# Kernel tuning notes

Measured on AMD Instinct MI355X. Metric: run time of the kernel, lower is better.

Reference implementation:

```python
import jax, jax.numpy as jnp
import numpy as np

N_NODES = 50000
N_EDGES = 800000
IN_F = 128
OUT_F = 128
EDGE_F = 6


def setup_inputs() -> dict:
    key = jax.random.key(0)
    k1, k2, k3, k4, k5, k6, k7 = jax.random.split(key, 7)
    nodeFeatures = jax.random.normal(k1, (N_NODES, IN_F), dtype=jnp.float32)
    edgeIndex = jax.random.randint(k2, (N_EDGES, 2), 0, N_NODES, dtype=jnp.int64)
    edgeFeatures = jax.random.normal(k3, (N_EDGES, EDGE_F), dtype=jnp.float32)
    # nn.Linear params (kaiming-uniform-ish init scale)
    lim_n = 1.0 / np.sqrt(IN_F)
    lim_e = 1.0 / np.sqrt(EDGE_F)
    W = jax.random.uniform(k4, (IN_F, OUT_F), minval=-lim_n, maxval=lim_n, dtype=jnp.float32)
    b = jax.random.uniform(k5, (OUT_F,), minval=-lim_n, maxval=lim_n, dtype=jnp.float32)
    We = jax.random.uniform(k6, (EDGE_F, OUT_F), minval=-lim_e, maxval=lim_e, dtype=jnp.float32)
    be = jax.random.uniform(k7, (OUT_F,), minval=-lim_e, maxval=lim_e, dtype=jnp.float32)
    return {"nodeFeatures": nodeFeatures, "edgeIndex": edgeIndex,
            "edgeFeatures": edgeFeatures, "W": W, "b": b, "We": We, "be": be}


def reference(nodeFeatures, edgeIndex, edgeFeatures, W, b, We, be):
    # node linear: [N, out]
    transformed = nodeFeatures @ W + b
    # edge linear: [E, out]
    edgeMsg = edgeFeatures @ We + be
    src = edgeIndex[:, 0]
    dst = edgeIndex[:, 1]
    # per-edge message = transformed[src] + edgeMsg, scatter-add into dst
    messages = transformed[src] + edgeMsg  # [E, out]
    aggregated = jax.ops.segment_sum(messages, dst, num_segments=nodeFeatures.shape[0])
    return jax.nn.relu(aggregated)
```

## Files before the change

kernel.cpp:

```cpp
#include <hip/hip_runtime.h>
#include <hip/hip_bf16.h>
#include <stdint.h>

#define IN_F 128
#define EDGE_F 6
#define TILE_E 4096
#define NBIN_PAD 256
#define BCAP 8192
#define IDXN 8192
#define CAST_B 400

using bf16x8 = __attribute__((ext_vector_type(8))) short;
using f32x4  = __attribute__((ext_vector_type(4))) float;

__device__ __forceinline__ float bf2f(unsigned short u) {
    return __uint_as_float(((unsigned int)u) << 16);
}
__device__ __forceinline__ unsigned short f2bfbits(float f) {
    __hip_bfloat16 h = __float2bfloat16(f);
    return *reinterpret_cast<unsigned short*>(&h);
}
__device__ __forceinline__ unsigned int packbf(float a, float b) {
    return ((unsigned int)f2bfbits(b) << 16) | (unsigned int)f2bfbits(a);
}

__global__ __launch_bounds__(256) void sort_pack_cast(
        const int* __restrict__ eidx, const float* __restrict__ ef,
        uint4* __restrict__ rec_c, unsigned short* __restrict__ pmat,
        unsigned short* __restrict__ lmat,
        int n_edges, int nblk_e, int n_cast, int n_nodes,
        const float* __restrict__ nf, unsigned short* __restrict__ nfb,
        const float* __restrict__ W, const float* __restrict__ b,
        const float* __restrict__ We, const float* __restrict__ be,
        unsigned short* __restrict__ Wpack, float* __restrict__ W2pack) {
    const int tid = threadIdx.x;
    const int blk = blockIdx.x;
    __shared__ unsigned int qxs[TILE_E];
    __shared__ int hist[NBIN_PAD];
    __shared__ int cur[NBIN_PAD];

    if (blk < nblk_e) {
        hist[tid] = 0;
        __syncthreads();
        const int e0 = blk * TILE_E;
        const int lim = min(TILE_E, n_edges - e0);
        for (int i = tid; i < lim; i += 256) {
            const int2 pr = reinterpret_cast<const int2*>(eidx)[e0 + i];
            const unsigned int q = (unsigned int)pr.x | ((unsigned int)pr.y << 16);
            qxs[i] = q;
            atomicAdd(&hist[q >> 24], 1);
        }
        __syncthreads();
        const int own = hist[tid];
        for (int off = 1; off < 256; off <<= 1) {
            int t2 = (tid >= off) ? hist[tid - off] : 0;
            __syncthreads();
            hist[tid] += t2;
            __syncthreads();
        }
        const int excl = hist[tid] - own;
        pmat[(size_t)blk * NBIN_PAD + tid] = (unsigned short)own;
        lmat[(size_t)blk * NBIN_PAD + tid] = (unsigned short)excl;
        cur[tid] = excl;
        __syncthreads();
        uint4* seg = rec_c + (size_t)blk * TILE_E;
        for (int i = tid; i < lim; i += 256) {
            const unsigned int q = qxs[i];
            const float2* efs = reinterpret_cast<const float2*>(ef + (size_t)(e0 + i) * EDGE_F);
            const float2 f0 = efs[0], f1 = efs[1], f2 = efs[2];
            uint4 r;
            r.x = q;
            r.y = packbf(f0.x, f0.y);
            r.z = packbf(f1.x, f1.y);
            r.w = packbf(f2.x, f2.y);
            const int pos = atomicAdd(&cur[q >> 24], 1);
            seg[pos] = r;
        }
    } else if (blk == nblk_e) {
        for (int idx = tid; idx < 16384; idx += 256) {
            int j = idx & 7, lane = (idx >> 3) & 63, ft = (idx >> 9) & 7, kb = idx >> 12;
            int k = kb * 32 + (lane >> 4) * 8 + j;
            int f = ft * 16 + (lane & 15);
            Wpack[idx] = f2bfbits(W[k * 128 + f]);
        }
        for (int idx = tid; idx < 1024; idx += 256) {
            int j = idx >> 7, f = idx & 127;
            float w = 0.f;
            if (j < 6)       w = We[j * 128 + f];
            else if (j == 6) w = b[f] + be[f];
            W2pack[idx] = w;
        }
        if (tid < 16) {
            uint4 z; z.x = z.y = z.z = z.w = 0u;
            reinterpret_cast<uint4*>(nfb + (size_t)n_nodes * IN_F)[tid] = z;
        }
    } else {
        const int cb = blk - nblk_e - 1;
        const int ncb = gridDim.x - nblk_e - 1;
        for (int i = cb * 256 + tid; i < n_cast; i += ncb * 256) {
            const float4 lo = reinterpret_cast<const float4*>(nf)[2 * i];
            const float4 hi = reinterpret_cast<const float4*>(nf)[2 * i + 1];
            uint4 o;
            o.x = packbf(lo.x, lo.y); o.y = packbf(lo.z, lo.w);
            o.z = packbf(hi.x, hi.y); o.w = packbf(hi.z, hi.w);
            reinterpret_cast<uint4*>(nfb)[i] = o;
        }
    }
}

__global__ __launch_bounds__(512) void fine_rank(
        const uint4* __restrict__ rec_c, const unsigned short* __restrict__ pmat,
        const unsigned short* __restrict__ lmat,
        uint4* __restrict__ rec, int2* __restrict__ pr2,
        int n_nodes, int nblk_e) {
    const int tid = threadIdx.x;
    const int c = blockIdx.x;
    __shared__ int rstart[NBIN_PAD + 1];
    __shared__ int rbaseg[NBIN_PAD];
    __shared__ int fcnt[256];
    __shared__ int fpos[256];
    __shared__ int idxl[IDXN];

    if (tid < 256) {
        const bool r = (tid < nblk_e);
        fcnt[tid] = r ? pmat[(size_t)tid * NBIN_PAD + c] : 0;
        rbaseg[tid] = tid * TILE_E + (r ? (int)lmat[(size_t)tid * NBIN_PAD + c] : 0);
    }
    __syncthreads();
    for (int off = 1; off < 256; off <<= 1) {
        int v = 0;
        if (tid < 256 && tid >= off) v = fcnt[tid - off];
        __syncthreads();
        if (tid < 256) fcnt[tid] += v;
        __syncthreads();
    }
    if (tid < 256) rstart[tid + 1] = fcnt[tid];
    if (tid == 0) rstart[0] = 0;
    __syncthreads();
    int sz = rstart[256];
    if (sz > IDXN) sz = IDXN;
    __syncthreads();
    if (tid < 256) fcnt[tid] = 0;
    __syncthreads();
    for (int base = 0; base < sz; base += 2048) {
        int ii[4], g[4];
        unsigned int qx[4];
#pragma unroll
        for (int u = 0; u < 4; ++u) ii[u] = base + u * 512 + tid;
#pragma unroll
        for (int u = 0; u < 4; ++u) {
            if (ii[u] < sz) {
                int lo = 0, hi = 255;
                while (lo < hi) {
                    const int mid = (lo + hi + 1) >> 1;
                    if (rstart[mid] <= ii[u]) lo = mid; else hi = mid - 1;
                }
                g[u] = rbaseg[lo] + (ii[u] - rstart[lo]);
                idxl[ii[u]] = g[u];
            }
        }
#pragma unroll
        for (int u = 0; u < 4; ++u)
            if (ii[u] < sz)
                qx[u] = reinterpret_cast<const unsigned int*>(rec_c)[(size_t)g[u] * 4];
#pragma unroll
        for (int u = 0; u < 4; ++u)
            if (ii[u] < sz) atomicAdd(&fcnt[(qx[u] >> 16) & 255], 1);
    }
    __syncthreads();
    int own = 0, ownp = 0, pexcl = 0;
    if (tid < 256) { own = fcnt[tid]; ownp = (own + 7) & ~7; fcnt[tid] = ownp; }
    __syncthreads();
    for (int off = 1; off < 256; off <<= 1) {
        int v = 0;
        if (tid < 256 && tid >= off) v = fcnt[tid - off];
        __syncthreads();
        if (tid < 256) fcnt[tid] += v;
        __syncthreads();
    }
    const size_t obase = (size_t)c * BCAP;
    if (tid < 256) {
        pexcl = fcnt[tid] - ownp;
        fpos[tid] = pexcl;
        const int n = c * 256 + tid;
        if (n < n_nodes) {
            int2 pr; pr.x = (int)(obase + pexcl); pr.y = own;
            pr2[n] = pr;
        }
    }
    __syncthreads();
    for (int base = 0; base < sz; base += 2048) {
        int ii[4];
        uint4 q[4];
#pragma unroll
        for (int u = 0; u < 4; ++u) ii[u] = base + u * 512 + tid;
#pragma unroll
        for (int u = 0; u < 4; ++u)
            if (ii[u] < sz) q[u] = rec_c[idxl[ii[u]]];
#pragma unroll
        for (int u = 0; u < 4; ++u) {
            if (ii[u] < sz) {
                const int r = atomicAdd(&fpos[(q[u].x >> 16) & 255], 1);
                if (r < BCAP) rec[obase + r] = q[u];
            }
        }
    }
    if (tid < 256) {
        uint4 dmy; dmy.x = (unsigned int)n_nodes; dmy.y = dmy.z = dmy.w = 0u;
        for (int j = own; j < ownp && pexcl + j < BCAP; ++j)
            rec[obase + pexcl + j] = dmy;
    }
}

__global__ __launch_bounds__(256) void aggregate_bf16(
        const unsigned short* __restrict__ nfb, const uint4* __restrict__ rec,
        const int2* __restrict__ pr2, unsigned short* __restrict__ S,
        unsigned short* __restrict__ E8, int n_nodes) {
    const int lane = threadIdx.x & 63;
    const int wv = __builtin_amdgcn_readfirstlane(threadIdx.x >> 6);
    const int n = blockIdx.x * 4 + wv;
    if (n >= n_nodes) return;
    const int2 pr = pr2[n];
    const int deg = pr.y;
    const int nb = (deg + 7) >> 3;
    const int half = lane >> 5;
    const int hl = lane & 31;
    float a0 = 0.f, a1 = 0.f, a2 = 0.f, a3 = 0.f;
    float e0 = 0.f, e1 = 0.f, e2 = 0.f, e3 = 0.f, e4 = 0.f, e5 = 0.f;
    int i = pr.x;
    for (int bb = 0; bb < nb; ++bb, i += 8) {
        uint4 q[8];
#pragma unroll
        for (int j = 0; j < 8; ++j) q[j] = rec[i + j];
        uint2 u[4];
#pragma unroll
        for (int p = 0; p < 4; ++p) {
            const unsigned int sA = q[2 * p].x & 0xFFFFu;
            const unsigned int sB = q[2 * p + 1].x & 0xFFFFu;
            const unsigned int s = half ? sB : sA;
            u[p] = reinterpret_cast<const uint2*>(nfb + (size_t)s * IN_F)[hl];
        }
#pragma unroll
        for (int p = 0; p < 4; ++p) {
            a0 += bf2f((unsigned short)u[p].x);
            a1 += bf2f((unsigned short)(u[p].x >> 16));
            a2 += bf2f((unsigned short)u[p].y);
            a3 += bf2f((unsigned short)(u[p].y >> 16));
        }
#pragma unroll
        for (int j = 0; j < 8; ++j) {
            e0 += bf2f((unsigned short)q[j].y);
            e1 += bf2f((unsigned short)(q[j].y >> 16));
            e2 += bf2f((unsigned short)q[j].z);
            e3 += bf2f((unsigned short)(q[j].z >> 16));
            e4 += bf2f((unsigned short)q[j].w);
            e5 += bf2f((unsigned short)(q[j].w >> 16));
        }
    }
    a0 += __shfl_xor(a0, 32, 64);
    a1 += __shfl_xor(a1, 32, 64);
    a2 += __shfl_xor(a2, 32, 64);
    a3 += __shfl_xor(a3, 32, 64);
    if (half == 0) {
        uint2 o;
        o.x = packbf(a0, a1);
        o.y = packbf(a2, a3);
        reinterpret_cast<uint2*>(S + (size_t)n * IN_F)[hl] = o;
    }
    if (lane == 0) {
        uint4 q;
        q.x = packbf(e0, e1);
        q.y = packbf(e2, e3);
        q.z = packbf(e4, e5);
        q.w = packbf((float)deg, 0.f);
        *reinterpret_cast<uint4*>(E8 + (size_t)n * 8) = q;
    }
}

__global__ __launch_bounds__(256) void gemm_mfma(
        const unsigned short* __restrict__ S, const unsigned short* __restrict__ E8,
        const unsigned short* __restrict__ Wpack, const float* __restrict__ W2pack,
        float* __restrict__ out, int n_nodes) {
    __shared__ __align__(16) short Wl[16384];
    __shared__ float W2l[1024];
    const int tid = threadIdx.x;
    for (int i = tid; i < 2048; i += 256)
        reinterpret_cast<uint4*>(Wl)[i] = reinterpret_cast<const uint4*>(Wpack)[i];
    for (int i = tid; i < 1024; i += 256) W2l[i] = W2pack[i];

    const int wv = tid >> 6, lane = tid & 63;
    const int m = lane & 15, quad = lane >> 4;
    const int n0 = blockIdx.x * 64 + wv * 16;

    const int arow = min(n0 + m, n_nodes - 1);
    const unsigned short* ap = S + (size_t)arow * IN_F + quad * 8;
    bf16x8 a[4];
#pragma unroll
    for (int kb = 0; kb < 4; ++kb)
        a[kb] = *reinterpret_cast<const bf16x8*>(ap + kb * 32);

    __syncthreads();

    f32x4 acc[8];
#pragma unroll
    for (int ft = 0; ft < 8; ++ft) acc[ft] = (f32x4){0.f, 0.f, 0.f, 0.f};

#pragma unroll
    for (int kb = 0; kb < 4; ++kb) {
#pragma unroll
        for (int ft = 0; ft < 8; ++ft) {
            const bf16x8 bfrag =
                reinterpret_cast<const bf16x8*>(Wl)[(kb * 8 + ft) * 64 + lane];
            acc[ft] = __builtin_amdgcn_mfma_f32_16x16x32_bf16(a[kb], bfrag, acc[ft], 0, 0, 0);
        }
    }

    float e[4][7];
#pragma unroll
    for (int r = 0; r < 4; ++r) {
        const int n = min(n0 + quad * 4 + r, n_nodes - 1);
        const uint4 q = *reinterpret_cast<const uint4*>(E8 + (size_t)n * 8);
        e[r][0] = bf2f((unsigned short)q.x); e[r][1] = bf2f((unsigned short)(q.x >> 16));
        e[r][2] = bf2f((unsigned short)q.y); e[r][3] = bf2f((unsigned short)(q.y >> 16));
        e[r][4] = bf2f((unsigned short)q.z); e[r][5] = bf2f((unsigned short)(q.z >> 16));
        e[r][6] = bf2f((unsigned short)q.w);
    }
    __syncthreads();
    float* So = reinterpret_cast<float*>(Wl);
#pragma unroll
    for (int ft = 0; ft < 8; ++ft) {
        const int f = ft * 16 + m;
        float w2[7];
#pragma unroll
        for (int j = 0; j < 7; ++j) w2[j] = W2l[j * 128 + f];
#pragma unroll
        for (int r = 0; r < 4; ++r) {
            float v = acc[ft][r];
#pragma unroll
            for (int j = 0; j < 7; ++j) v += e[r][j] * w2[j];
            So[(wv * 16 + quad * 4 + r) * 128 + f] = fmaxf(v, 0.f);
        }
    }
    __syncthreads();
    const size_t nb0 = (size_t)blockIdx.x * 64;
    for (int i = tid; i < 2048; i += 256) {
        const int row = i >> 5;
        if (nb0 + row < (size_t)n_nodes)
            reinterpret_cast<uint4*>(out)[(nb0 + row) * 32 + (i & 31)] =
                reinterpret_cast<const uint4*>(So)[i];
    }
}

extern "C" void kernel_launch(void* const* d_in, const int* in_sizes, int n_in,
                              void* d_out, int out_size, void* d_ws, size_t ws_size,
                              hipStream_t stream) {
    const float* nf = (const float*)d_in[0];
    const int* eidx = (const int*)d_in[1];
    const float* ef = (const float*)d_in[2];
    const float* W  = (const float*)d_in[3];
    const float* b  = (const float*)d_in[4];
    const float* We = (const float*)d_in[5];
    const float* be = (const float*)d_in[6];
    float* out = (float*)d_out;

    const int n_nodes = in_sizes[0] / IN_F;
    const int n_edges = in_sizes[1] / 2;

    const int nblk_e = (n_edges + TILE_E - 1) / TILE_E;
    const int nbin = (n_nodes + 255) >> 8;
    const int n_cast = n_nodes * (IN_F / 8);

    uint4* rec   = (uint4*)d_ws;
    uint4* rec_c = rec + (size_t)nbin * BCAP;
    unsigned short* S = (unsigned short*)(rec_c + (size_t)nblk_e * TILE_E);
    unsigned short* E8 = S + (size_t)n_nodes * IN_F;
    unsigned short* Wpack = E8 + (size_t)n_nodes * 8;
    float* W2pack = (float*)(Wpack + 16384);
    int2* pr2 = (int2*)(W2pack + 1024);
    unsigned short* pmat = (unsigned short*)(pr2 + n_nodes);
    unsigned short* lmat = pmat + (size_t)nblk_e * NBIN_PAD;
    unsigned short* nfb = lmat + (size_t)nblk_e * NBIN_PAD;

    sort_pack_cast<<<nblk_e + 1 + CAST_B, 256, 0, stream>>>(
        eidx, ef, rec_c, pmat, lmat, n_edges, nblk_e, n_cast, n_nodes,
        nf, nfb, W, b, We, be, Wpack, W2pack);
    fine_rank<<<nbin, 512, 0, stream>>>(rec_c, pmat, lmat, rec, pr2,
                                        n_nodes, nblk_e);
    aggregate_bf16<<<(n_nodes + 3) / 4, 256, 0, stream>>>(nfb, rec, pr2, S, E8, n_nodes);
    gemm_mfma<<<(n_nodes + 63) / 64, 256, 0, stream>>>(S, E8, Wpack, W2pack, out, n_nodes);
}
```

Measured before the change: 177.6 us.

## Split bf16 node table into four feature-quarter passes for cache-resident gathers

The bf16 node-feature table is stored as four column-quarter tables of 32 features each, and aggregation runs four passes, each gathering only one quarter. A single quarter table is a quarter of the full table's size, so the random source-row gathers are more likely to hit in L2/MALL. A compact 16-bit source-index array is also written so the later passes do not reread the 16-byte edge records; only pass 0 accumulates edge features. The cost is four times as many aggregate blocks, a repeated CSR walk with narrower 8-byte gathers per pass, a three-stage shuffle reduction, and extra index-array writes in the ranking kernel.

```diff
diff --git a/kernel.cpp b/kernel.cpp
--- a/kernel.cpp
+++ b/kernel.cpp
@@ -28,13 +28,14 @@
         const int* __restrict__ eidx, const float* __restrict__ ef,
         uint4* __restrict__ rec_c, unsigned short* __restrict__ pmat,
         unsigned short* __restrict__ lmat,
-        int n_edges, int nblk_e, int n_cast, int n_nodes,
-        const float* __restrict__ nf, unsigned short* __restrict__ nfb,
+        int n_edges, int nblk_e, int n_nodes,
+        const float* __restrict__ nf, unsigned short* __restrict__ nfbq,
         const float* __restrict__ W, const float* __restrict__ b,
         const float* __restrict__ We, const float* __restrict__ be,
         unsigned short* __restrict__ Wpack, float* __restrict__ W2pack) {
     const int tid = threadIdx.x;
     const int blk = blockIdx.x;
+    const size_t qstr = (size_t)(n_nodes + 1) * 32;
     __shared__ unsigned int qxs[TILE_E];
     __shared__ int hist[NBIN_PAD];
     __shared__ int cur[NBIN_PAD];
@@ -91,19 +92,29 @@
             W2pack[idx] = w;
         }
         if (tid < 16) {
+            const int q = tid >> 2, sub = tid & 3;
             uint4 z; z.x = z.y = z.z = z.w = 0u;
-            reinterpret_cast<uint4*>(nfb + (size_t)n_nodes * IN_F)[tid] = z;
+            *reinterpret_cast<uint4*>(nfbq + (size_t)q * qstr +
+                                      (size_t)n_nodes * 32 + sub * 8) = z;
         }
     } else {
         const int cb = blk - nblk_e - 1;
         const int ncb = gridDim.x - nblk_e - 1;
-        for (int i = cb * 256 + tid; i < n_cast; i += ncb * 256) {
-            const float4 lo = reinterpret_cast<const float4*>(nf)[2 * i];
-            const float4 hi = reinterpret_cast<const float4*>(nf)[2 * i + 1];
+        const int per_q = n_nodes * 4;
+        const int total = n_nodes * 16;
+        for (int i = cb * 256 + tid; i < total; i += ncb * 256) {
+            const int q = i / per_q;
+            const int rem = i - q * per_q;
+            const int node = rem >> 2, sub = rem & 3;
+            const float4 lo = *reinterpret_cast<const float4*>(
+                nf + (size_t)node * IN_F + q * 32 + sub * 8);
+            const float4 hi = *reinterpret_cast<const float4*>(
+                nf + (size_t)node * IN_F + q * 32 + sub * 8 + 4);
             uint4 o;
             o.x = packbf(lo.x, lo.y); o.y = packbf(lo.z, lo.w);
             o.z = packbf(hi.x, hi.y); o.w = packbf(hi.z, hi.w);
-            reinterpret_cast<uint4*>(nfb)[i] = o;
+            *reinterpret_cast<uint4*>(nfbq + (size_t)q * qstr +
+                                      (size_t)node * 32 + sub * 8) = o;
         }
     }
 }
@@ -111,8 +122,8 @@
 __global__ __launch_bounds__(512) void fine_rank(
         const uint4* __restrict__ rec_c, const unsigned short* __restrict__ pmat,
         const unsigned short* __restrict__ lmat,
-        uint4* __restrict__ rec, int2* __restrict__ pr2,
-        int n_nodes, int nblk_e) {
+        uint4* __restrict__ rec, unsigned short* __restrict__ srcp,
+        int2* __restrict__ pr2, int n_nodes, int nblk_e) {
     const int tid = threadIdx.x;
     const int c = blockIdx.x;
     __shared__ int rstart[NBIN_PAD + 1];
@@ -201,73 +212,79 @@
         for (int u = 0; u < 4; ++u) {
             if (ii[u] < sz) {
                 const int r = atomicAdd(&fpos[(q[u].x >> 16) & 255], 1);
-                if (r < BCAP) rec[obase + r] = q[u];
+                if (r < BCAP) {
+                    rec[obase + r] = q[u];
+                    srcp[obase + r] = (unsigned short)(q[u].x & 0xFFFFu);
+                }
             }
         }
     }
     if (tid < 256) {
         uint4 dmy; dmy.x = (unsigned int)n_nodes; dmy.y = dmy.z = dmy.w = 0u;
-        for (int j = own; j < ownp && pexcl + j < BCAP; ++j)
+        for (int j = own; j < ownp && pexcl + j < BCAP; ++j) {
             rec[obase + pexcl + j] = dmy;
+            srcp[obase + pexcl + j] = (unsigned short)n_nodes;
+        }
     }
 }
 
 __global__ __launch_bounds__(256) void aggregate_bf16(
-        const unsigned short* __restrict__ nfb, const uint4* __restrict__ rec,
-        const int2* __restrict__ pr2, unsigned short* __restrict__ S,
-        unsigned short* __restrict__ E8, int n_nodes) {
+        const unsigned short* __restrict__ nfbq, const uint4* __restrict__ rec,
+        const unsigned short* __restrict__ srcp, const int2* __restrict__ pr2,
+        unsigned short* __restrict__ Sq, unsigned short* __restrict__ E8,
+        int n_nodes, int nbn) {
     const int lane = threadIdx.x & 63;
     const int wv = __builtin_amdgcn_readfirstlane(threadIdx.x >> 6);
-    const int n = blockIdx.x * 4 + wv;
+    const int pass = blockIdx.x / nbn;
+    const int bi = blockIdx.x - pass * nbn;
+    const int n = bi * 4 + wv;
     if (n >= n_nodes) return;
+    const size_t qstr = (size_t)(n_nodes + 1) * 32;
+    const unsigned short* tab = nfbq + (size_t)pass * qstr;
     const int2 pr = pr2[n];
     const int deg = pr.y;
     const int nb = (deg + 7) >> 3;
-    const int half = lane >> 5;
-    const int hl = lane & 31;
-    float a0 = 0.f, a1 = 0.f, a2 = 0.f, a3 = 0.f;
+    const int es = lane >> 3;
+    const int fl = lane & 7;
+    float b0 = 0.f, b1 = 0.f, b2 = 0.f, b3 = 0.f;
     float e0 = 0.f, e1 = 0.f, e2 = 0.f, e3 = 0.f, e4 = 0.f, e5 = 0.f;
     int i = pr.x;
     for (int bb = 0; bb < nb; ++bb, i += 8) {
-        uint4 q[8];
-#pragma unroll
-        for (int j = 0; j < 8; ++j) q[j] = rec[i + j];
-        uint2 u[4];
-#pragma unroll
-        for (int p = 0; p < 4; ++p) {
-            const unsigned int sA = q[2 * p].x & 0xFFFFu;
-            const unsigned int sB = q[2 * p + 1].x & 0xFFFFu;
-            const unsigned int s = half ? sB : sA;
-            u[p] = reinterpret_cast<const uint2*>(nfb + (size_t)s * IN_F)[hl];
-        }
-#pragma unroll
-        for (int p = 0; p < 4; ++p) {
-            a0 += bf2f((unsigned short)u[p].x);
-            a1 += bf2f((unsigned short)(u[p].x >> 16));
-            a2 += bf2f((unsigned short)u[p].y);
-            a3 += bf2f((unsigned short)(u[p].y >> 16));
-        }
-#pragma unroll
-        for (int j = 0; j < 8; ++j) {
-            e0 += bf2f((unsigned short)q[j].y);
-            e1 += bf2f((unsigned short)(q[j].y >> 16));
-            e2 += bf2f((unsigned short)q[j].z);
-            e3 += bf2f((unsigned short)(q[j].z >> 16));
-            e4 += bf2f((unsigned short)q[j].w);
-            e5 += bf2f((unsigned short)(q[j].w >> 16));
-        }
-    }
-    a0 += __shfl_xor(a0, 32, 64);
-    a1 += __shfl_xor(a1, 32, 64);
-    a2 += __shfl_xor(a2, 32, 64);
-    a3 += __shfl_xor(a3, 32, 64);
-    if (half == 0) {
+        const int s = srcp[i + es];
+        const uint2 u = *reinterpret_cast<const uint2*>(tab + (size_t)s * 32 + fl * 4);
+        b0 += bf2f((unsigned short)u.x);
+        b1 += bf2f((unsigned short)(u.x >> 16));
+        b2 += bf2f((unsigned short)u.y);
+        b3 += bf2f((unsigned short)(u.y >> 16));
+        if (pass == 0) {
+            uint4 q[8];
+#pragma unroll
+            for (int j = 0; j < 8; ++j) q[j] = rec[i + j];
+#pragma unroll
+            for (int j = 0; j < 8; ++j) {
+                e0 += bf2f((unsigned short)q[j].y);
+                e1 += bf2f((unsigned short)(q[j].y >> 16));
+                e2 += bf2f((unsigned short)q[j].z);
+                e3 += bf2f((unsigned short)(q[j].z >> 16));
+                e4 += bf2f((unsigned short)q[j].w);
+                e5 += bf2f((unsigned short)(q[j].w >> 16));
+            }
+        }
+    }
+    b0 += __shfl_xor(b0, 8, 64);  b1 += __shfl_xor(b1, 8, 64);
+    b2 += __shfl_xor(b2, 8, 64);  b3 += __shfl_xor(b3, 8, 64);
+    b0 += __shfl_xor(b0, 16, 64); b1 += __shfl_xor(b1, 16, 64);
+    b2 += __shfl_xor(b2, 16, 64); b3 += __shfl_xor(b3, 16, 64);
+    b0 += __shfl_xor(b0, 32, 64); b1 += __shfl_xor(b1, 32, 64);
+    b2 += __shfl_xor(b2, 32, 64); b3 += __shfl_xor(b3, 32, 64);
+    if (es == 0) {
         uint2 o;
-        o.x = packbf(a0, a1);
-        o.y = packbf(a2, a3);
-        reinterpret_cast<uint2*>(S + (size_t)n * IN_F)[hl] = o;
-    }
-    if (lane == 0) {
+        o.x = packbf(b0, b1);
+        o.y = packbf(b2, b3);
+        *reinterpret_cast<uint2*>(Sq + (size_t)pass * n_nodes * 32 +
+                                  (size_t)n * 32 + fl * 4) = o;
+    }
+    if (pass == 0 && lane == 0) {
         uint4 q;
         q.x = packbf(e0, e1);
         q.y = packbf(e2, e3);
@@ -278,7 +295,7 @@
 }
 
 __global__ __launch_bounds__(256) void gemm_mfma(
-        const unsigned short* __restrict__ S, const unsigned short* __restrict__ E8,
+        const unsigned short* __restrict__ Sq, const unsigned short* __restrict__ E8,
         const unsigned short* __restrict__ Wpack, const float* __restrict__ W2pack,
         float* __restrict__ out, int n_nodes) {
     __shared__ __align__(16) short Wl[16384];
@@ -293,11 +310,11 @@
     const int n0 = blockIdx.x * 64 + wv * 16;
 
     const int arow = min(n0 + m, n_nodes - 1);
-    const unsigned short* ap = S + (size_t)arow * IN_F + quad * 8;
     bf16x8 a[4];
 #pragma unroll
     for (int kb = 0; kb < 4; ++kb)
-        a[kb] = *reinterpret_cast<const bf16x8*>(ap + kb * 32);
+        a[kb] = *reinterpret_cast<const bf16x8*>(
+            Sq + (size_t)kb * n_nodes * 32 + (size_t)arow * 32 + quad * 8);
 
     __syncthreads();
 
@@ -368,24 +385,26 @@
 
     const int nblk_e = (n_edges + TILE_E - 1) / TILE_E;
     const int nbin = (n_nodes + 255) >> 8;
-    const int n_cast = n_nodes * (IN_F / 8);
+    const int nbn = (n_nodes + 3) / 4;
 
     uint4* rec   = (uint4*)d_ws;
     uint4* rec_c = rec + (size_t)nbin * BCAP;
-    unsigned short* S = (unsigned short*)(rec_c + (size_t)nblk_e * TILE_E);
-    unsigned short* E8 = S + (size_t)n_nodes * IN_F;
+    unsigned short* E8 = (unsigned short*)(rec_c + (size_t)nblk_e * TILE_E);
     unsigned short* Wpack = E8 + (size_t)n_nodes * 8;
-    float* W2pack = (float*)(Wpack + 16384);
+    unsigned short* Sq = Wpack + 16384;
+    unsigned short* nfbq = Sq + (size_t)4 * n_nodes * 32;
+    unsigned short* srcp = nfbq + (size_t)4 * (n_nodes + 1) * 32;
+    unsigned short* pmat = srcp + (size_t)nbin * BCAP;
+    unsigned short* lmat = pmat + (size_t)nblk_e * NBIN_PAD;
+    float* W2pack = (float*)(lmat + (size_t)nblk_e * NBIN_PAD);
     int2* pr2 = (int2*)(W2pack + 1024);
-    unsigned short* pmat = (unsigned short*)(pr2 + n_nodes);
-    unsigned short* lmat = pmat + (size_t)nblk_e * NBIN_PAD;
-    unsigned short* nfb = lmat + (size_t)nblk_e * NBIN_PAD;
 
     sort_pack_cast<<<nblk_e + 1 + CAST_B, 256, 0, stream>>>(
-        eidx, ef, rec_c, pmat, lmat, n_edges, nblk_e, n_cast, n_nodes,
-        nf, nfb, W, b, We, be, Wpack, W2pack);
-    fine_rank<<<nbin, 512, 0, stream>>>(rec_c, pmat, lmat, rec, pr2,
+        eidx, ef, rec_c, pmat, lmat, n_edges, nblk_e, n_nodes,
+        nf, nfbq, W, b, We, be, Wpack, W2pack);
+    fine_rank<<<nbin, 512, 0, stream>>>(rec_c, pmat, lmat, rec, srcp, pr2,
                                         n_nodes, nblk_e);
-    aggregate_bf16<<<(n_nodes + 3) / 4, 256, 0, stream>>>(nfb, rec, pr2, S, E8, n_nodes);
-    gemm_mfma<<<(n_nodes + 63) / 64, 256, 0, stream>>>(S, E8, Wpack, W2pack, out, n_nodes);
-}
+    aggregate_bf16<<<4 * nbn, 256, 0, stream>>>(nfbq, rec, srcp, pr2, Sq, E8,
+                                                n_nodes, nbn);
+    gemm_mfma<<<(n_nodes + 63) / 64, 256, 0, stream>>>(Sq, E8, Wpack, W2pack, out, n_nodes);
+}
```

Result: slower. 232.4 us (+30.9%).
